# Optimization experiments

Measured on AMD Instinct MI355X. Metric: run time of the kernel, lower is better.

The kernel has to match this reference:

```python
import jax, jax.numpy as jnp
import numpy as np

N = 100000      # nodes
E = 1000000     # edges (before self-loops)
F_IN = 128
HID = 64
OUT = 40
L = 4           # n_layers (GCNII conv layers)
ALPHA = 0.5
EPS = 1e-5      # BatchNorm eps


def setup_inputs() -> dict:
    key = jax.random.key(0)
    ks = jax.random.split(key, 8)
    x = jax.random.normal(ks[0], (N, F_IN), dtype=jnp.float32)
    edge_index = jax.random.randint(ks[1], (2, E), 0, N, dtype=jnp.int64)
    # glorot-ish scales
    Wi = jax.random.normal(ks[2], (F_IN, HID), dtype=jnp.float32) / np.sqrt(F_IN)
    bi = jnp.zeros((HID,), dtype=jnp.float32)
    w1 = jax.random.normal(ks[3], (L, HID, HID), dtype=jnp.float32) / np.sqrt(HID)
    w2 = jax.random.normal(ks[4], (L, HID, HID), dtype=jnp.float32) / np.sqrt(HID)
    gamma = jnp.ones((L, HID), dtype=jnp.float32)
    beta = jnp.zeros((L, HID), dtype=jnp.float32)
    Wo = jax.random.normal(ks[5], (HID, OUT), dtype=jnp.float32) / np.sqrt(HID)
    bo = jnp.zeros((OUT,), dtype=jnp.float32)
    return {"x": x, "edge_index": edge_index, "Wi": Wi, "bi": bi,
            "w1": w1, "w2": w2, "gamma": gamma, "beta": beta,
            "Wo": Wo, "bo": bo}


def _gcn_norm(edge_index):
    # add self loops, weight 1; deg scattered onto col (PyG gcn_norm)
    loop = jnp.arange(N, dtype=edge_index.dtype)
    row = jnp.concatenate([edge_index[0], loop])
    col = jnp.concatenate([edge_index[1], loop])
    ew = jnp.ones((E + N,), dtype=jnp.float32)
    deg = jax.ops.segment_sum(ew, col, num_segments=N)
    dinv = jnp.where(deg > 0, deg ** -0.5, 0.0)
    norm = dinv[row] * ew * dinv[col]
    return row, col, norm


def _bn(h, g, b):
    # BatchNorm1d in training mode: batch stats, biased variance
    m = h.mean(axis=0)
    v = h.var(axis=0)
    return g * (h - m) * jax.lax.rsqrt(v + EPS) + b


def reference(x, edge_index, Wi, bi, w1, w2, gamma, beta, Wo, bo):
    row, col, norm = _gcn_norm(edge_index)

    h = jax.nn.relu(x @ Wi + bi)          # [N, HID]
    h0 = h
    hprev = h
    for l in range(L):
        support = hprev + hprev @ w1[l]                    # x + x W1
        initial = ALPHA * h0 + h0 @ w2[l]                  # alpha h0 + h0 W2
        msg = norm[:, None] * support[row]                 # [E+N, HID] edge messages
        agg = jax.ops.segment_sum(msg, col, num_segments=N)
        out = _bn(agg + initial, gamma[l], beta[l])
        hprev = jax.nn.relu(out) + hprev                   # residual to previous hidden
    return hprev @ Wo + bo                                 # [N, OUT]
```

## Files before the change

kernel.cpp:

```cpp
#include <hip/hip_runtime.h>

#define N_NODES 100000
#define E_EDGES 1000000
#define F_IN    128
#define HID     64
#define OUT_F   40
#define LAYERS  4
#define ALPHA   0.5f
#define BN_EPS  1e-5f

#define SCAN_BLOCKS ((N_NODES + 255) / 256)
#define TILE_BLOCKS ((N_NODES + 63) / 64)

typedef __attribute__((ext_vector_type(8))) short short8;
typedef __attribute__((ext_vector_type(4))) float f32x4;

__device__ inline unsigned short f2bf(float f) {
    union { float f; unsigned u; } v; v.f = f;
    unsigned r = v.u + 0x7FFFu + ((v.u >> 16) & 1u);
    return (unsigned short)(r >> 16);
}
__device__ inline float bf2f(unsigned short s) {
    union { unsigned u; float f; } v; v.u = ((unsigned)s) << 16;
    return v.f;
}

__global__ __launch_bounds__(256) void k_deg_count(const int* __restrict__ col,
                                                   int* __restrict__ degInt) {
    int e = blockIdx.x * 256 + threadIdx.x;
    if (e < E_EDGES) atomicAdd(&degInt[col[e]], 1);
}

__global__ __launch_bounds__(256) void k_scanA(const int* __restrict__ degInt,
                                               int* __restrict__ tmpIncl,
                                               int* __restrict__ blockSums) {
    __shared__ int sm[256];
    int i = blockIdx.x * 256 + threadIdx.x;
    int v = (i < N_NODES) ? degInt[i] : 0;
    sm[threadIdx.x] = v;
    __syncthreads();
    for (int d = 1; d < 256; d <<= 1) {
        int t = (threadIdx.x >= d) ? sm[threadIdx.x - d] : 0;
        __syncthreads();
        sm[threadIdx.x] += t;
        __syncthreads();
    }
    if (i < N_NODES) tmpIncl[i] = sm[threadIdx.x];
    if (threadIdx.x == 255) blockSums[blockIdx.x] = sm[255];
}

__global__ __launch_bounds__(512) void k_scanB(int* __restrict__ blockSums,
                                               int* __restrict__ blockOff) {
    __shared__ int sm[512];
    int t = threadIdx.x;
    int v = (t < SCAN_BLOCKS) ? blockSums[t] : 0;
    sm[t] = v;
    __syncthreads();
    for (int d = 1; d < 512; d <<= 1) {
        int u = (t >= d) ? sm[t - d] : 0;
        __syncthreads();
        sm[t] += u;
        __syncthreads();
    }
    if (t < SCAN_BLOCKS) blockOff[t] = sm[t] - v;
}

__global__ __launch_bounds__(256) void k_scanC(const int* __restrict__ degInt,
                                               const int* __restrict__ tmpIncl,
                                               const int* __restrict__ blockOff,
                                               int* __restrict__ rowOff,
                                               int* __restrict__ cursor,
                                               float* __restrict__ dinv) {
    int i = blockIdx.x * 256 + threadIdx.x;
    if (i >= N_NODES) return;
    int d = degInt[i];
    int incl = tmpIncl[i] + blockOff[blockIdx.x];
    int excl = incl - d;
    rowOff[i] = excl;
    cursor[i] = excl;
    dinv[i] = rsqrtf((float)(d + 1));
    if (i == N_NODES - 1) rowOff[N_NODES] = incl;
}

__global__ __launch_bounds__(256) void k_fill(const int* __restrict__ ei,
                                              int* __restrict__ cursor,
                                              int* __restrict__ srow) {
    int e = blockIdx.x * 256 + threadIdx.x;
    if (e >= E_EDGES) return;
    int r = ei[e];
    int c = ei[E_EDGES + e];
    int pos = atomicAdd(&cursor[c], 1);
    srow[pos] = r;
}

__global__ __launch_bounds__(256) void k_input(const float* __restrict__ x,
                                               const float* __restrict__ Wi,
                                               const float* __restrict__ bi,
                                               unsigned short* __restrict__ h0bf,
                                               float* __restrict__ hprev) {
    __shared__ __align__(16) unsigned short xb[64 * 136];
    __shared__ __align__(16) unsigned short wib[64 * 136];
    __shared__ float bis[64];
    const int tid = threadIdx.x;
    const int n0 = blockIdx.x * 64;
    const int nvalid = min(64, N_NODES - n0);

    if (tid < 64) bis[tid] = bi[tid];
    for (int i = tid; i < F_IN * HID; i += 256) {
        int k = i >> 6, j = i & 63;
        wib[j * 136 + k] = f2bf(Wi[i]);
    }
    for (int i = tid; i < 64 * F_IN; i += 256) {
        int node = i >> 7, k = i & 127;
        float v = (node < nvalid) ? x[(size_t)(n0 + node) * F_IN + k] : 0.0f;
        xb[node * 136 + k] = f2bf(v);
    }
    __syncthreads();

    const int lane = tid & 63, wid = tid >> 6;
    const int ml = lane & 15, gl = lane >> 4;
    const int r0 = wid * 16;

    short8 A[4];
    #pragma unroll
    for (int ks = 0; ks < 4; ++ks)
        A[ks] = *(const short8*)&xb[(r0 + ml) * 136 + ks * 32 + gl * 8];

    #pragma unroll
    for (int ct = 0; ct < 4; ++ct) {
        f32x4 z = {0.f, 0.f, 0.f, 0.f};
        #pragma unroll
        for (int ks = 0; ks < 4; ++ks) {
            short8 b = *(const short8*)&wib[(ct * 16 + ml) * 136 + ks * 32 + gl * 8];
            z = __builtin_amdgcn_mfma_f32_16x16x32_bf16(A[ks], b, z, 0, 0, 0);
        }
        #pragma unroll
        for (int reg = 0; reg < 4; ++reg) {
            int node = n0 + r0 + gl * 4 + reg;
            if (node < N_NODES) {
                int col = ct * 16 + ml;
                float h = fmaxf(z[reg] + bis[col], 0.0f);
                int gidx = node * HID + col;
                h0bf[gidx]  = f2bf(h);
                hprev[gidx] = h;
            }
        }
    }
}

__global__ __launch_bounds__(256) void k_layerA(float* __restrict__ hprev,
                                                const unsigned short* __restrict__ h0bf,
                                                float* __restrict__ agg,
                                                const float* __restrict__ sums_prev,
                                                const float* __restrict__ gamma,
                                                const float* __restrict__ beta,
                                                int apply_bn,
                                                const float* __restrict__ w1g,
                                                const float* __restrict__ w2g,
                                                const float* __restrict__ dinv,
                                                unsigned short* __restrict__ sscaled) {
    __shared__ float hp_lds[64 * 68];
    __shared__ __align__(16) unsigned short wt1[64 * 72];
    __shared__ __align__(16) unsigned short wt2[64 * 72];
    const int tid = threadIdx.x;
    const int n0 = blockIdx.x * 64;

    for (int i = tid; i < HID * HID; i += 256) {
        int k = i >> 6, j = i & 63;
        wt1[j * 72 + k] = f2bf(w1g[i]);
        wt2[j * 72 + k] = f2bf(w2g[i]);
    }

    const int feat = tid & 63;
    const float invN = 1.0f / (float)N_NODES;
    float m = 0.f, inv = 0.f, gam = 0.f, bet = 0.f;
    if (apply_bn) {
        float mm = sums_prev[feat] * invN;
        float vv = sums_prev[HID + feat] * invN - mm * mm;
        m = mm; inv = rsqrtf(vv + BN_EPS);
        gam = gamma[feat]; bet = beta[feat];
    }
    const int nvalid = min(64, N_NODES - n0);
    for (int idx = tid; idx < 64 * HID; idx += 256) {
        int node = idx >> 6;
        float hp = 0.0f;
        if (node < nvalid) {
            int g = (n0 + node) * HID + feat;
            hp = hprev[g];
            if (apply_bn) {
                float a = agg[g];
                hp += fmaxf(gam * (a - m) * inv + bet, 0.0f);
                hprev[g] = hp;
            }
        }
        hp_lds[node * 68 + feat] = hp;
    }
    __syncthreads();

    const int lane = tid & 63, wid = tid >> 6;
    const int ml = lane & 15, gl = lane >> 4;
    const int r0 = wid * 16;

    short8 A1[2], A2[2];
    #pragma unroll
    for (int ks = 0; ks < 2; ++ks) {
        const f32x4* p = (const f32x4*)&hp_lds[(r0 + ml) * 68 + ks * 32 + gl * 8];
        f32x4 x0 = p[0], x1 = p[1];
        short8 fr;
        fr[0] = f2bf(x0[0]); fr[1] = f2bf(x0[1]); fr[2] = f2bf(x0[2]); fr[3] = f2bf(x0[3]);
        fr[4] = f2bf(x1[0]); fr[5] = f2bf(x1[1]); fr[6] = f2bf(x1[2]); fr[7] = f2bf(x1[3]);
        A1[ks] = fr;
        A2[ks] = *(const short8*)&h0bf[(size_t)(n0 + r0 + ml) * HID + ks * 32 + gl * 8];
    }

    f32x4 acc1[4], acc2[4];
    #pragma unroll
    for (int ct = 0; ct < 4; ++ct) {
        short8 b10 = *(const short8*)&wt1[(ct * 16 + ml) * 72 + gl * 8];
        short8 b11 = *(const short8*)&wt1[(ct * 16 + ml) * 72 + 32 + gl * 8];
        short8 b20 = *(const short8*)&wt2[(ct * 16 + ml) * 72 + gl * 8];
        short8 b21 = *(const short8*)&wt2[(ct * 16 + ml) * 72 + 32 + gl * 8];
        f32x4 z = {0.f, 0.f, 0.f, 0.f};
        z = __builtin_amdgcn_mfma_f32_16x16x32_bf16(A1[0], b10, z, 0, 0, 0);
        z = __builtin_amdgcn_mfma_f32_16x16x32_bf16(A1[1], b11, z, 0, 0, 0);
        acc1[ct] = z;
        f32x4 y = {0.f, 0.f, 0.f, 0.f};
        y = __builtin_amdgcn_mfma_f32_16x16x32_bf16(A2[0], b20, y, 0, 0, 0);
        y = __builtin_amdgcn_mfma_f32_16x16x32_bf16(A2[1], b21, y, 0, 0, 0);
        acc2[ct] = y;
    }

    #pragma unroll
    for (int reg = 0; reg < 4; ++reg) {
        int i = gl * 4 + reg;
        int node = n0 + r0 + i;
        if (node < N_NODES) {
            float dv = dinv[node];
            #pragma unroll
            for (int ct = 0; ct < 4; ++ct) {
                int col = ct * 16 + ml;
                int gidx = node * HID + col;
                float hp = hp_lds[(r0 + i) * 68 + col];
                float hz = bf2f(h0bf[gidx]);
                float s   = hp + acc1[ct][reg];
                float ini = ALPHA * hz + acc2[ct][reg];
                float ss  = dv * s;
                sscaled[gidx] = f2bf(ss);
                agg[gidx] = ini + dv * ss;
            }
        }
    }
}

__global__ __launch_bounds__(256) void k_gather(const int* __restrict__ rowOff,
                                                const int* __restrict__ srow,
                                                const float* __restrict__ dinv,
                                                const unsigned short* __restrict__ sscaled,
                                                float* __restrict__ agg,
                                                float* __restrict__ sums) {
    __shared__ float ls[4][HID];
    __shared__ float lq[4][HID];
    int lane = threadIdx.x & 63, w = threadIdx.x >> 6;
    int wg = blockIdx.x * 4 + w;
    int nw = gridDim.x * 4;
    float s = 0.0f, q = 0.0f;
    for (int n = wg; n < N_NODES; n += nw) {
        int o0 = rowOff[n], o1 = rowOff[n + 1];
        float acc0 = 0.0f, acc1 = 0.0f, acc2 = 0.0f, acc3 = 0.0f;
        int e = o0;
        for (; e + 4 <= o1; e += 4) {
            int r0 = srow[e], r1 = srow[e + 1], r2 = srow[e + 2], r3 = srow[e + 3];
            acc0 += bf2f(sscaled[(size_t)r0 * HID + lane]);
            acc1 += bf2f(sscaled[(size_t)r1 * HID + lane]);
            acc2 += bf2f(sscaled[(size_t)r2 * HID + lane]);
            acc3 += bf2f(sscaled[(size_t)r3 * HID + lane]);
        }
        for (; e < o1; ++e) {
            int r = srow[e];
            acc0 += bf2f(sscaled[(size_t)r * HID + lane]);
        }
        float dv = dinv[n];
        size_t idx = (size_t)n * HID + lane;
        float a = agg[idx] + dv * ((acc0 + acc1) + (acc2 + acc3));
        agg[idx] = a;
        s += a;
        q = fmaf(a, a, q);
    }
    ls[w][lane] = s;
    lq[w][lane] = q;
    __syncthreads();
    if (threadIdx.x < HID) {
        float ts = ls[0][lane] + ls[1][lane] + ls[2][lane] + ls[3][lane];
        float tq = lq[0][lane] + lq[1][lane] + lq[2][lane] + lq[3][lane];
        atomicAdd(&sums[lane], ts);
        atomicAdd(&sums[HID + lane], tq);
    }
}

__global__ __launch_bounds__(256) void k_out(const float* __restrict__ hprev,
                                             const float* __restrict__ agg,
                                             const float* __restrict__ sums,
                                             const float* __restrict__ gamma,
                                             const float* __restrict__ beta,
                                             const float* __restrict__ Wo,
                                             const float* __restrict__ bo,
                                             float* __restrict__ out) {
    __shared__ __align__(16) unsigned short hb[64 * 72];
    __shared__ __align__(16) unsigned short wot[48 * 72];
    __shared__ float bos[48];
    const int tid = threadIdx.x;
    const int n0 = blockIdx.x * 64;
    const int nvalid = min(64, N_NODES - n0);

    for (int i = tid; i < 48 * 72; i += 256) wot[i] = 0;
    if (tid < 48) bos[tid] = (tid < OUT_F) ? bo[tid] : 0.0f;
    __syncthreads();
    for (int i = tid; i < HID * OUT_F; i += 256) {
        int k = i / OUT_F, j = i % OUT_F;
        wot[j * 72 + k] = f2bf(Wo[i]);
    }

    const int feat = tid & 63;
    const float invN = 1.0f / (float)N_NODES;
    float mm = sums[feat] * invN;
    float vv = sums[HID + feat] * invN - mm * mm;
    float inv = rsqrtf(vv + BN_EPS);
    float g = gamma[feat], b = beta[feat];
    for (int idx = tid; idx < 64 * HID; idx += 256) {
        int node = idx >> 6;
        float h = 0.0f;
        if (node < nvalid) {
            int gi = (n0 + node) * HID + feat;
            float a = agg[gi];
            h = hprev[gi] + fmaxf(g * (a - mm) * inv + b, 0.0f);
        }
        hb[node * 72 + feat] = f2bf(h);
    }
    __syncthreads();

    const int lane = tid & 63, wid = tid >> 6;
    const int ml = lane & 15, gl = lane >> 4;
    const int r0 = wid * 16;

    short8 A0 = *(const short8*)&hb[(r0 + ml) * 72 + gl * 8];
    short8 A1 = *(const short8*)&hb[(r0 + ml) * 72 + 32 + gl * 8];

    #pragma unroll
    for (int ct = 0; ct < 3; ++ct) {
        short8 b0 = *(const short8*)&wot[(ct * 16 + ml) * 72 + gl * 8];
        short8 b1 = *(const short8*)&wot[(ct * 16 + ml) * 72 + 32 + gl * 8];
        f32x4 z = {0.f, 0.f, 0.f, 0.f};
        z = __builtin_amdgcn_mfma_f32_16x16x32_bf16(A0, b0, z, 0, 0, 0);
        z = __builtin_amdgcn_mfma_f32_16x16x32_bf16(A1, b1, z, 0, 0, 0);
        int col = ct * 16 + ml;
        #pragma unroll
        for (int reg = 0; reg < 4; ++reg) {
            int node = n0 + r0 + gl * 4 + reg;
            if (node < N_NODES && col < OUT_F)
                out[(size_t)node * OUT_F + col] = z[reg] + bos[col];
        }
    }
}

extern "C" void kernel_launch(void* const* d_in, const int* in_sizes, int n_in,
                              void* d_out, int out_size, void* d_ws, size_t ws_size,
                              hipStream_t stream) {
    const float* x     = (const float*)d_in[0];
    const int*   ei    = (const int*)  d_in[1];
    const float* Wi    = (const float*)d_in[2];
    const float* bi    = (const float*)d_in[3];
    const float* w1    = (const float*)d_in[4];
    const float* w2    = (const float*)d_in[5];
    const float* gamma = (const float*)d_in[6];
    const float* beta  = (const float*)d_in[7];
    const float* Wo    = (const float*)d_in[8];
    const float* bo    = (const float*)d_in[9];
    float* out = (float*)d_out;

    char* ws = (char*)d_ws;
    const size_t NH  = (size_t)N_NODES * HID * sizeof(float);
    const size_t NHB = (size_t)N_NODES * HID * sizeof(unsigned short);
    size_t off = 0;
    auto alloc = [&](size_t bytes) { void* p = ws + off; off += (bytes + 255) & ~255UL; return p; };
    int*   degInt    = (int*)  alloc(N_NODES * sizeof(int));
    int*   tmpIncl   = (int*)  alloc(N_NODES * sizeof(int));
    int*   blockSums = (int*)  alloc(SCAN_BLOCKS * sizeof(int));
    int*   blockOff  = (int*)  alloc(SCAN_BLOCKS * sizeof(int));
    int*   rowOff    = (int*)  alloc((N_NODES + 1) * sizeof(int));
    int*   cursor    = (int*)  alloc(N_NODES * sizeof(int));
    int*   srow      = (int*)  alloc(E_EDGES * sizeof(int));
    float* dinv      = (float*)alloc(N_NODES * sizeof(float));
    unsigned short* sscaled = (unsigned short*)alloc(NHB);
    unsigned short* h0bf    = (unsigned short*)alloc(NHB);
    float* agg       = (float*)alloc(NH);
    float* hprev     = (float*)alloc(NH);
    float* sums      = (float*)alloc(LAYERS * 128 * sizeof(float));
    (void)ws_size; (void)in_sizes; (void)n_in; (void)out_size;

    hipMemsetAsync(degInt, 0, N_NODES * sizeof(int), stream);
    hipMemsetAsync(sums, 0, LAYERS * 128 * sizeof(float), stream);

    k_deg_count<<<(E_EDGES + 255) / 256, 256, 0, stream>>>(ei + E_EDGES, degInt);
    k_scanA<<<SCAN_BLOCKS, 256, 0, stream>>>(degInt, tmpIncl, blockSums);
    k_scanB<<<1, 512, 0, stream>>>(blockSums, blockOff);
    k_scanC<<<SCAN_BLOCKS, 256, 0, stream>>>(degInt, tmpIncl, blockOff,
                                             rowOff, cursor, dinv);
    k_fill<<<(E_EDGES + 255) / 256, 256, 0, stream>>>(ei, cursor, srow);

    k_input<<<TILE_BLOCKS, 256, 0, stream>>>(x, Wi, bi, h0bf, hprev);

    for (int l = 0; l < LAYERS; ++l) {
        const float* sums_prev = (l > 0) ? (sums + (l - 1) * 128) : sums;
        const float* gm        = (l > 0) ? (gamma + (l - 1) * HID) : gamma;
        const float* bt        = (l > 0) ? (beta  + (l - 1) * HID) : beta;
        k_layerA<<<TILE_BLOCKS, 256, 0, stream>>>(hprev, h0bf, agg,
                                                  sums_prev, gm, bt, (l > 0),
                                                  w1 + (size_t)l * HID * HID,
                                                  w2 + (size_t)l * HID * HID,
                                                  dinv, sscaled);
        k_gather<<<2048, 256, 0, stream>>>(rowOff, srow, dinv, sscaled, agg,
                                           sums + l * 128);
    }

    k_out<<<TILE_BLOCKS, 256, 0, stream>>>(hprev, agg, sums + 3 * 128,
                                           gamma + 3 * HID, beta + 3 * HID, Wo, bo, out);
}
```

Baseline: 748.6 us.

## Gather neighbor rows with 8-lane groups using 16-byte vector loads

```diff
diff --git a/kernel.cpp b/kernel.cpp
--- a/kernel.cpp
+++ b/kernel.cpp
@@ -14,6 +14,7 @@
 
 typedef __attribute__((ext_vector_type(8))) short short8;
 typedef __attribute__((ext_vector_type(4))) float f32x4;
+typedef __attribute__((ext_vector_type(8))) unsigned short ushort8v;
 
 __device__ inline unsigned short f2bf(float f) {
     union { float f; unsigned u; } v; v.f = f;
@@ -258,42 +259,67 @@
                                                 const unsigned short* __restrict__ sscaled,
                                                 float* __restrict__ agg,
                                                 float* __restrict__ sums) {
-    __shared__ float ls[4][HID];
-    __shared__ float lq[4][HID];
-    int lane = threadIdx.x & 63, w = threadIdx.x >> 6;
-    int wg = blockIdx.x * 4 + w;
-    int nw = gridDim.x * 4;
-    float s = 0.0f, q = 0.0f;
-    for (int n = wg; n < N_NODES; n += nw) {
+    __shared__ float lsum[HID];
+    __shared__ float lqsum[HID];
+    const int tid = threadIdx.x;
+    if (tid < HID) { lsum[tid] = 0.0f; lqsum[tid] = 0.0f; }
+    __syncthreads();
+
+    const int ml = tid & 7;
+    const int gid = (blockIdx.x * 256 + tid) >> 3;
+    const int ngrp = (gridDim.x * 256) >> 3;
+    f32x4 s0 = {0.f,0.f,0.f,0.f}, s1 = {0.f,0.f,0.f,0.f};
+    f32x4 q0 = {0.f,0.f,0.f,0.f}, q1 = {0.f,0.f,0.f,0.f};
+
+    for (int n = gid; n < N_NODES; n += ngrp) {
         int o0 = rowOff[n], o1 = rowOff[n + 1];
-        float acc0 = 0.0f, acc1 = 0.0f, acc2 = 0.0f, acc3 = 0.0f;
+        f32x4 aA0 = {0.f,0.f,0.f,0.f}, aA1 = {0.f,0.f,0.f,0.f};
+        f32x4 aB0 = {0.f,0.f,0.f,0.f}, aB1 = {0.f,0.f,0.f,0.f};
         int e = o0;
-        for (; e + 4 <= o1; e += 4) {
-            int r0 = srow[e], r1 = srow[e + 1], r2 = srow[e + 2], r3 = srow[e + 3];
-            acc0 += bf2f(sscaled[(size_t)r0 * HID + lane]);
-            acc1 += bf2f(sscaled[(size_t)r1 * HID + lane]);
-            acc2 += bf2f(sscaled[(size_t)r2 * HID + lane]);
-            acc3 += bf2f(sscaled[(size_t)r3 * HID + lane]);
-        }
-        for (; e < o1; ++e) {
+        for (; e + 2 <= o1; e += 2) {
+            int r0 = srow[e], r1 = srow[e + 1];
+            ushort8v a = *(const ushort8v*)&sscaled[(size_t)r0 * HID + ml * 8];
+            ushort8v b = *(const ushort8v*)&sscaled[(size_t)r1 * HID + ml * 8];
+            aA0[0] += bf2f(a[0]); aA0[1] += bf2f(a[1]); aA0[2] += bf2f(a[2]); aA0[3] += bf2f(a[3]);
+            aA1[0] += bf2f(a[4]); aA1[1] += bf2f(a[5]); aA1[2] += bf2f(a[6]); aA1[3] += bf2f(a[7]);
+            aB0[0] += bf2f(b[0]); aB0[1] += bf2f(b[1]); aB0[2] += bf2f(b[2]); aB0[3] += bf2f(b[3]);
+            aB1[0] += bf2f(b[4]); aB1[1] += bf2f(b[5]); aB1[2] += bf2f(b[6]); aB1[3] += bf2f(b[7]);
+        }
+        if (e < o1) {
             int r = srow[e];
-            acc0 += bf2f(sscaled[(size_t)r * HID + lane]);
+            ushort8v a = *(const ushort8v*)&sscaled[(size_t)r * HID + ml * 8];
+            aA0[0] += bf2f(a[0]); aA0[1] += bf2f(a[1]); aA0[2] += bf2f(a[2]); aA0[3] += bf2f(a[3]);
+            aA1[0] += bf2f(a[4]); aA1[1] += bf2f(a[5]); aA1[2] += bf2f(a[6]); aA1[3] += bf2f(a[7]);
         }
         float dv = dinv[n];
-        size_t idx = (size_t)n * HID + lane;
-        float a = agg[idx] + dv * ((acc0 + acc1) + (acc2 + acc3));
-        agg[idx] = a;
-        s += a;
-        q = fmaf(a, a, q);
-    }
-    ls[w][lane] = s;
-    lq[w][lane] = q;
-    __syncthreads();
-    if (threadIdx.x < HID) {
-        float ts = ls[0][lane] + ls[1][lane] + ls[2][lane] + ls[3][lane];
-        float tq = lq[0][lane] + lq[1][lane] + lq[2][lane] + lq[3][lane];
-        atomicAdd(&sums[lane], ts);
-        atomicAdd(&sums[HID + lane], tq);
+        float* ap = &agg[(size_t)n * HID + ml * 8];
+        f32x4 x0 = *(const f32x4*)ap;
+        f32x4 x1 = *(const f32x4*)(ap + 4);
+        #pragma unroll
+        for (int j = 0; j < 4; ++j) {
+            x0[j] += dv * (aA0[j] + aB0[j]);
+            x1[j] += dv * (aA1[j] + aB1[j]);
+        }
+        *(f32x4*)ap = x0;
+        *(f32x4*)(ap + 4) = x1;
+        #pragma unroll
+        for (int j = 0; j < 4; ++j) {
+            s0[j] += x0[j];  q0[j] = fmaf(x0[j], x0[j], q0[j]);
+            s1[j] += x1[j];  q1[j] = fmaf(x1[j], x1[j], q1[j]);
+        }
+    }
+
+    #pragma unroll
+    for (int j = 0; j < 4; ++j) {
+        atomicAdd(&lsum[ml * 8 + j], s0[j]);
+        atomicAdd(&lsum[ml * 8 + 4 + j], s1[j]);
+        atomicAdd(&lqsum[ml * 8 + j], q0[j]);
+        atomicAdd(&lqsum[ml * 8 + 4 + j], q1[j]);
+    }
+    __syncthreads();
+    if (tid < HID) {
+        atomicAdd(&sums[tid], lsum[tid]);
+        atomicAdd(&sums[HID + tid], lqsum[tid]);
     }
 }
 
```

Measured after the change: 719.1 us. 1.04x faster.
